# Kernel optimization log

Measured on AMD Instinct MI355X. Metric: run time of the kernel, lower is better.

Reference implementation:

```python
import jax, jax.numpy as jnp
import numpy as np

N_NODES = 100000
N_EDGES = 1600000
IN_CH = 128
HID = 128
OUT_DIM = 1
N_LAYERS = 3
N_GRAPHS = 512


def setup_inputs() -> dict:
    key = jax.random.key(0)
    ks = jax.random.split(key, 12)
    x = jax.random.normal(ks[0], (N_NODES, IN_CH), dtype=jnp.float32)
    edge_index = jax.random.randint(ks[1], (2, N_EDGES), 0, N_NODES, dtype=jnp.int64)
    batch = jnp.sort(jax.random.randint(ks[2], (N_NODES,), 0, N_GRAPHS, dtype=jnp.int64))
    # GCNConv weights (glorot) and biases; layer 0: in->hid, rest hid->hid (all 128x128 here)
    def glorot(k, fan_in, fan_out):
        lim = jnp.sqrt(6.0 / (fan_in + fan_out)).astype(jnp.float32)
        return jax.random.uniform(k, (fan_in, fan_out), jnp.float32, -lim, lim)
    Ws = jnp.stack([glorot(ks[3 + i], IN_CH if i == 0 else HID, HID) for i in range(N_LAYERS)])
    bs = jnp.zeros((N_LAYERS, HID), dtype=jnp.float32)
    head_w = glorot(ks[8], HID, OUT_DIM)  # stored as [hid, out] == head_weight.T
    head_b = jnp.zeros((OUT_DIM,), dtype=jnp.float32)
    return {"x": x, "edge_index": edge_index, "batch": batch,
            "Ws": Ws, "bs": bs, "head_w": head_w, "head_b": head_b}


def _gcn_norm(edge_index, n_nodes):
    # PyG gcn_norm: add self-loops, deg over dst, norm = d^-1/2[src]*d^-1/2[dst]
    loops = jnp.arange(n_nodes, dtype=edge_index.dtype)
    src = jnp.concatenate([edge_index[0], loops])
    dst = jnp.concatenate([edge_index[1], loops])
    deg = jax.ops.segment_sum(jnp.ones_like(dst, dtype=jnp.float32), dst, num_segments=n_nodes)
    dinv = jnp.where(deg > 0, jax.lax.rsqrt(deg), 0.0)
    norm = dinv[src] * dinv[dst]
    return src, dst, norm


def reference(x, edge_index, batch, Ws, bs, head_w, head_b):
    n = x.shape[0]
    src, dst, norm = _gcn_norm(edge_index, n)
    h = x.astype(jnp.float32)
    for i in range(N_LAYERS):
        t = h @ Ws[i]                                   # [N, hid]
        msg = t[src] * norm[:, None]                    # gather + scale [E+N, hid]
        h = jax.ops.segment_sum(msg, dst, num_segments=n) + bs[i]
        h = jax.nn.relu(h)                              # dropout p=0 -> identity
    g = jax.ops.segment_sum(h, batch, num_segments=N_GRAPHS)  # global_add_pool
    out = g @ head_w + head_b                           # [G, 1]
    return out.reshape(-1)                              # squeeze out_dim==1
```

## Files before the change

kernel.cpp:

```cpp
#include <hip/hip_runtime.h>

#define NN 100000
#define NE 1600000
#define CH 128
#define NG 512
#define NL 3
#define BSZ 512
#define NBUK ((NN + BSZ - 1) / BSZ)
#define TILE 4096

typedef short bf8 __attribute__((ext_vector_type(8)));
typedef float f4 __attribute__((ext_vector_type(4)));
typedef unsigned int u32x4 __attribute__((ext_vector_type(4)));
typedef unsigned short u16;
typedef unsigned int u32;

__device__ __forceinline__ long long ld_idx(const void* p, long long i, bool is64) {
    return is64 ? ((const long long*)p)[i] : (long long)((const int*)p)[i];
}
__device__ __forceinline__ u16 f2bf(float f) {
    u32 u = __float_as_uint(f);
    u += 0x7fffu + ((u >> 16) & 1u);
    return (u16)(u >> 16);
}
__device__ __forceinline__ float bflo(u32 v) { return __uint_as_float(v << 16); }
__device__ __forceinline__ float bfhi(u32 v) { return __uint_as_float(v & 0xffff0000u); }

__global__ void k_zero(int* bcnt, int* flags) {
    int i = blockIdx.x * blockDim.x + threadIdx.x;
    if (i < NBUK) bcnt[i] = 0;
    if (i < 2) flags[i] = 0;
}

__global__ void k_detect(const int* __restrict__ ei32, const int* __restrict__ b32, int* flags) {
    int acc_e = 0, acc_b = 0;
    long long stride = (long long)gridDim.x * blockDim.x;
    long long t0 = (long long)blockIdx.x * blockDim.x + threadIdx.x;
    for (long long i = t0; i < (1 << 18); i += stride) acc_e |= ei32[2 * i + 1];
    for (long long i = t0; i < NN / 2; i += stride) acc_b |= b32[2 * i + 1];
    if (acc_e) atomicOr(&flags[0], 1);
    if (acc_b) atomicOr(&flags[1], 1);
}


__global__ __launch_bounds__(256) void k_hist(const void* __restrict__ ei,
                                              const int* __restrict__ flags,
                                              int* __restrict__ bcnt) {
    __shared__ int cnt[NBUK];
    int tid = threadIdx.x;
    long long e0 = (long long)blockIdx.x * TILE;
    bool is64 = (flags[0] == 0);
    for (int b = tid; b < NBUK; b += 256) cnt[b] = 0;
    __syncthreads();
#pragma unroll
    for (int k = 0; k < 16; ++k) {
        long long e = e0 + tid + k * 256;
        if (e < NE) {
            int d = (int)ld_idx(ei, NE + e, is64);
            atomicAdd(&cnt[d >> 9], 1);
        }
    }
    __syncthreads();
    for (int b = tid; b < NBUK; b += 256)
        if (cnt[b]) atomicAdd(&bcnt[b], cnt[b]);
}

__global__ __launch_bounds__(256) void k_bscan(const int* __restrict__ bcnt,
                                               int* __restrict__ gbase,
                                               int* __restrict__ gcur,
                                               int* __restrict__ rowptr) {
    __shared__ int ws4[4];
    int t = threadIdx.x;
    int v = (t < NBUK) ? bcnt[t] : 0;
    int x = v;
#pragma unroll
    for (int d = 1; d < 64; d <<= 1) {
        int y = __shfl_up(x, d, 64);
        if ((t & 63) >= d) x += y;
    }
    if ((t & 63) == 63) ws4[t >> 6] = x;
    __syncthreads();
    if (t == 0) {
        int s = 0;
#pragma unroll
        for (int w = 0; w < 4; ++w) { int tmp = ws4[w]; ws4[w] = s; s += tmp; }
    }
    __syncthreads();
    int ex = x - v + ws4[t >> 6];
    if (t < NBUK) { gbase[t] = ex; gcur[t] = ex; }
    if (t == NBUK - 1) gbase[NBUK] = ex + v;
    if (t == 0) rowptr[NN] = NE;
}

__global__ __launch_bounds__(256) void k_bin(const void* __restrict__ ei,
                                             const int* __restrict__ flags,
                                             int* __restrict__ gcur,
                                             u32* __restrict__ bin) {
    __shared__ u32 stag[TILE];
    __shared__ int cnt[NBUK], loff[NBUK], lcur[NBUK], gb_s[NBUK];
    int tid = threadIdx.x;
    long long e0 = (long long)blockIdx.x * TILE;
    bool is64 = (flags[0] == 0);

    u32 rec[16];
    int bk[16];
#pragma unroll
    for (int k = 0; k < 16; ++k) {
        long long e = e0 + tid + k * 256;
        if (e < NE) {
            int s = (int)ld_idx(ei, e, is64);
            int d = (int)ld_idx(ei, NE + e, is64);
            rec[k] = ((u32)s << 9) | (u32)(d & (BSZ - 1));
            bk[k] = d >> 9;
        } else bk[k] = -1;
    }
    for (int b = tid; b < NBUK; b += 256) { cnt[b] = 0; lcur[b] = 0; }
    __syncthreads();
#pragma unroll
    for (int k = 0; k < 16; ++k)
        if (bk[k] >= 0) atomicAdd(&cnt[bk[k]], 1);
    __syncthreads();
    if (tid == 0) {
        int run = 0;
        for (int b = 0; b < NBUK; ++b) { loff[b] = run; run += cnt[b]; }
    }
    __syncthreads();
    if (tid < NBUK && cnt[tid] > 0) gb_s[tid] = atomicAdd(&gcur[tid], cnt[tid]);
    __syncthreads();
#pragma unroll
    for (int k = 0; k < 16; ++k)
        if (bk[k] >= 0) {
            int pos = loff[bk[k]] + atomicAdd(&lcur[bk[k]], 1);
            stag[pos] = rec[k];
        }
    __syncthreads();
    int wv = tid >> 6, lane = tid & 63;
    for (int b = wv; b < NBUK; b += 4) {
        int n = cnt[b];
        int gb = (n > 0) ? gb_s[b] : 0;
        int lo = loff[b];
        for (int j = lane; j < n; j += 64) bin[gb + j] = stag[lo + j];
    }
}

__global__ __launch_bounds__(512) void k_fillc(const u32* __restrict__ bin,
                                               const int* __restrict__ gbase,
                                               int* __restrict__ rowptr,
                                               float* __restrict__ dinv,
                                               u32* __restrict__ csr) {
    __shared__ int cnt[BSZ];
    __shared__ int lcur[BSZ];
    __shared__ int wsum[8];
    int b = blockIdx.x, tid = threadIdx.x;
    int gb = gbase[b], ge = gbase[b + 1];
    cnt[tid] = 0;
    __syncthreads();
    for (int i = gb + tid; i < ge; i += BSZ)
        atomicAdd(&cnt[bin[i] & (BSZ - 1)], 1);
    __syncthreads();
    int v = cnt[tid];
    int x = v;
#pragma unroll
    for (int d = 1; d < 64; d <<= 1) {
        int y = __shfl_up(x, d, 64);
        if ((tid & 63) >= d) x += y;
    }
    if ((tid & 63) == 63) wsum[tid >> 6] = x;
    __syncthreads();
    if (tid == 0) {
        int s = 0;
#pragma unroll
        for (int w = 0; w < 8; ++w) { int tmp = wsum[w]; wsum[w] = s; s += tmp; }
    }
    __syncthreads();
    int off = gb + x - v + wsum[tid >> 6];
    int node = b * BSZ + tid;
    if (node < NN) {
        rowptr[node] = off;
        dinv[node] = rsqrtf((float)v + 1.0f);
    }
    lcur[tid] = off;
    __syncthreads();
    for (int i = gb + tid; i < ge; i += BSZ) {
        u32 rec = bin[i];
        int pos = atomicAdd(&lcur[rec & (BSZ - 1)], 1);
        csr[pos] = rec >> 9;
    }
}

__global__ void k_cvt_w(const float* __restrict__ Ws, u16* __restrict__ Wt) {
    int j = (blockIdx.x * blockDim.x + threadIdx.x) * 4;
    if (j >= NL * CH * CH) return;
    int l = j >> 14, c = (j >> 7) & 127, k = j & 127;
    ushort4 o;
    o.x = f2bf(Ws[(l << 14) + ((k + 0) << 7) + c]);
    o.y = f2bf(Ws[(l << 14) + ((k + 1) << 7) + c]);
    o.z = f2bf(Ws[(l << 14) + ((k + 2) << 7) + c]);
    o.w = f2bf(Ws[(l << 14) + ((k + 3) << 7) + c]);
    *(ushort4*)(Wt + j) = o;
}

template <int F32IN>
__global__ __launch_bounds__(256) void k_mm_t(const void* __restrict__ Ain,
                                              const u16* __restrict__ Wt,
                                              u16* __restrict__ out) {
    int tid = threadIdx.x;
    int lane = tid & 63;
    int wv = tid >> 6;
    int rbase = blockIdx.x * 128 + wv * 32;
    int lm = lane & 15;
    int lk = (lane >> 4) << 3;

    f4 acc[2][8];
#pragma unroll
    for (int m = 0; m < 2; ++m)
#pragma unroll
        for (int n = 0; n < 8; ++n) acc[m][n] = (f4){0.f, 0.f, 0.f, 0.f};

    int r0 = rbase + lm;      if (r0 >= NN) r0 = NN - 1;
    int r1 = rbase + 16 + lm; if (r1 >= NN) r1 = NN - 1;

#pragma unroll
    for (int kk = 0; kk < 4; ++kk) {
        int ko = kk * 32 + lk;
        bf8 a0, a1;
        if (F32IN) {
            const float* A = (const float*)Ain;
            float4 p0 = *(const float4*)(A + (size_t)r0 * CH + ko);
            float4 q0 = *(const float4*)(A + (size_t)r0 * CH + ko + 4);
            float4 p1 = *(const float4*)(A + (size_t)r1 * CH + ko);
            float4 q1 = *(const float4*)(A + (size_t)r1 * CH + ko + 4);
            a0[0] = (short)f2bf(p0.x); a0[1] = (short)f2bf(p0.y);
            a0[2] = (short)f2bf(p0.z); a0[3] = (short)f2bf(p0.w);
            a0[4] = (short)f2bf(q0.x); a0[5] = (short)f2bf(q0.y);
            a0[6] = (short)f2bf(q0.z); a0[7] = (short)f2bf(q0.w);
            a1[0] = (short)f2bf(p1.x); a1[1] = (short)f2bf(p1.y);
            a1[2] = (short)f2bf(p1.z); a1[3] = (short)f2bf(p1.w);
            a1[4] = (short)f2bf(q1.x); a1[5] = (short)f2bf(q1.y);
            a1[6] = (short)f2bf(q1.z); a1[7] = (short)f2bf(q1.w);
        } else {
            const u16* A = (const u16*)Ain;
            a0 = *(const bf8*)(A + (size_t)r0 * CH + ko);
            a1 = *(const bf8*)(A + (size_t)r1 * CH + ko);
        }
#pragma unroll
        for (int n = 0; n < 8; ++n) {
            bf8 b = *(const bf8*)(Wt + (n * 16 + lm) * CH + ko);
            acc[0][n] = __builtin_amdgcn_mfma_f32_16x16x32_bf16(a0, b, acc[0][n], 0, 0, 0);
            acc[1][n] = __builtin_amdgcn_mfma_f32_16x16x32_bf16(a1, b, acc[1][n], 0, 0, 0);
        }
    }

#pragma unroll
    for (int m = 0; m < 2; ++m) {
        int rb = rbase + m * 16 + (lane >> 4) * 4;
#pragma unroll
        for (int r = 0; r < 4; ++r) {
            int row = rb + r;
            if (row < NN) {
#pragma unroll
                for (int n = 0; n < 8; ++n)
                    out[(size_t)row * CH + n * 16 + lm] = f2bf(acc[m][n][r]);
            }
        }
    }
}

#define ACC8W(v, w) \
    acc[0] = fmaf(bflo(v[0]), w, acc[0]); acc[1] = fmaf(bfhi(v[0]), w, acc[1]); \
    acc[2] = fmaf(bflo(v[1]), w, acc[2]); acc[3] = fmaf(bfhi(v[1]), w, acc[3]); \
    acc[4] = fmaf(bflo(v[2]), w, acc[4]); acc[5] = fmaf(bfhi(v[2]), w, acc[5]); \
    acc[6] = fmaf(bflo(v[3]), w, acc[6]); acc[7] = fmaf(bfhi(v[3]), w, acc[7]);

__global__ __launch_bounds__(256) void k_aggr(const u16* __restrict__ t,
                                              const int* __restrict__ rowptr,
                                              const u32* __restrict__ csr,
                                              const float* __restrict__ dinv,
                                              const float* __restrict__ b,
                                              u16* __restrict__ h,
                                              const float* __restrict__ hw,
                                              float* __restrict__ partial) {
    int node = blockIdx.x * 16 + (threadIdx.x >> 4);
    if (node >= NN) return;
    int l16 = threadIdx.x & 15;
    int c8 = l16 << 3;
    const u32x4* tp = (const u32x4*)t;

    int beg = rowptr[node], end = rowptr[node + 1];
    float dn = dinv[node];
    float acc[8];
#pragma unroll
    for (int k = 0; k < 8; ++k) acc[k] = 0.f;

    int j = beg;
    for (; j + 8 <= end; j += 8) {
        int s0 = (int)csr[j],     s1 = (int)csr[j + 1];
        int s2 = (int)csr[j + 2], s3 = (int)csr[j + 3];
        int s4 = (int)csr[j + 4], s5 = (int)csr[j + 5];
        int s6 = (int)csr[j + 6], s7 = (int)csr[j + 7];
        float w0 = dinv[s0], w1 = dinv[s1], w2 = dinv[s2], w3 = dinv[s3];
        float w4 = dinv[s4], w5 = dinv[s5], w6 = dinv[s6], w7 = dinv[s7];
        u32x4 v0 = tp[s0 * 16 + l16];
        u32x4 v1 = tp[s1 * 16 + l16];
        u32x4 v2 = tp[s2 * 16 + l16];
        u32x4 v3 = tp[s3 * 16 + l16];
        u32x4 v4 = tp[s4 * 16 + l16];
        u32x4 v5 = tp[s5 * 16 + l16];
        u32x4 v6 = tp[s6 * 16 + l16];
        u32x4 v7 = tp[s7 * 16 + l16];
        ACC8W(v0, w0); ACC8W(v1, w1); ACC8W(v2, w2); ACC8W(v3, w3);
        ACC8W(v4, w4); ACC8W(v5, w5); ACC8W(v6, w6); ACC8W(v7, w7);
    }
    for (; j + 4 <= end; j += 4) {
        int s0 = (int)csr[j], s1 = (int)csr[j + 1];
        int s2 = (int)csr[j + 2], s3 = (int)csr[j + 3];
        float w0 = dinv[s0], w1 = dinv[s1], w2 = dinv[s2], w3 = dinv[s3];
        u32x4 v0 = tp[s0 * 16 + l16];
        u32x4 v1 = tp[s1 * 16 + l16];
        u32x4 v2 = tp[s2 * 16 + l16];
        u32x4 v3 = tp[s3 * 16 + l16];
        ACC8W(v0, w0); ACC8W(v1, w1); ACC8W(v2, w2); ACC8W(v3, w3);
    }
    for (; j < end; ++j) {
        int s = (int)csr[j];
        float w = dinv[s];
        u32x4 v = tp[s * 16 + l16];
        ACC8W(v, w);
    }

    u32x4 sv = tp[node * 16 + l16];
    float4 b0 = *(const float4*)(b + c8);
    float4 b1 = *(const float4*)(b + c8 + 4);
    float r[8];
    r[0] = fmaxf(fmaf(fmaf(bflo(sv[0]), dn, acc[0]), dn, b0.x), 0.f);
    r[1] = fmaxf(fmaf(fmaf(bfhi(sv[0]), dn, acc[1]), dn, b0.y), 0.f);
    r[2] = fmaxf(fmaf(fmaf(bflo(sv[1]), dn, acc[2]), dn, b0.z), 0.f);
    r[3] = fmaxf(fmaf(fmaf(bfhi(sv[1]), dn, acc[3]), dn, b0.w), 0.f);
    r[4] = fmaxf(fmaf(fmaf(bflo(sv[2]), dn, acc[4]), dn, b1.x), 0.f);
    r[5] = fmaxf(fmaf(fmaf(bfhi(sv[2]), dn, acc[5]), dn, b1.y), 0.f);
    r[6] = fmaxf(fmaf(fmaf(bflo(sv[3]), dn, acc[6]), dn, b1.z), 0.f);
    r[7] = fmaxf(fmaf(fmaf(bfhi(sv[3]), dn, acc[7]), dn, b1.w), 0.f);

    if (hw) {
        float4 w0 = *(const float4*)(hw + c8);
        float4 w1 = *(const float4*)(hw + c8 + 4);
        float d = r[0] * w0.x + r[1] * w0.y + r[2] * w0.z + r[3] * w0.w
                + r[4] * w1.x + r[5] * w1.y + r[6] * w1.z + r[7] * w1.w;
#pragma unroll
        for (int off = 8; off > 0; off >>= 1) d += __shfl_xor(d, off);
        if (l16 == 0) partial[node] = d;
    } else {
        u32x4 o;
        o[0] = ((u32)f2bf(r[1]) << 16) | (u32)f2bf(r[0]);
        o[1] = ((u32)f2bf(r[3]) << 16) | (u32)f2bf(r[2]);
        o[2] = ((u32)f2bf(r[5]) << 16) | (u32)f2bf(r[4]);
        o[3] = ((u32)f2bf(r[7]) << 16) | (u32)f2bf(r[6]);
        ((u32x4*)h)[node * 16 + l16] = o;
    }
}


__device__ __forceinline__ int lbound(const void* bt, bool is64, int target) {
    int lo = 0, hi = NN;
    while (lo < hi) {
        int mid = (lo + hi) >> 1;
        long long v = ld_idx(bt, mid, is64);
        if (v < (long long)target) lo = mid + 1; else hi = mid;
    }
    return lo;
}

__global__ __launch_bounds__(256) void k_head(const float* __restrict__ partial,
                                              const void* __restrict__ batch,
                                              const int* __restrict__ flags,
                                              const float* __restrict__ hb,
                                              float* __restrict__ out) {
    int g = blockIdx.x * 4 + (threadIdx.x >> 6);
    if (g >= NG) return;
    int lane = threadIdx.x & 63;
    bool is64 = (flags[1] == 0);
    int lo = lbound(batch, is64, g);
    int hi = lbound(batch, is64, g + 1);
    float s = 0.f;
    for (int i = lo + lane; i < hi; i += 64) s += partial[i];
#pragma unroll
    for (int off = 32; off > 0; off >>= 1) s += __shfl_down(s, off);
    if (lane == 0) out[g] = s + hb[0];
}

extern "C" void kernel_launch(void* const* d_in, const int* in_sizes, int n_in,
                              void* d_out, int out_size, void* d_ws, size_t ws_size,
                              hipStream_t stream) {
    const float* x  = (const float*)d_in[0];
    const void*  ei = d_in[1];
    const void*  bt = d_in[2];
    const float* Ws = (const float*)d_in[3];
    const float* bs = (const float*)d_in[4];
    const float* hw = (const float*)d_in[5];
    const float* hb = (const float*)d_in[6];
    float* out = (float*)d_out;

    char* ws = (char*)d_ws;
    size_t p = 0;
    auto alloc = [&](size_t bytes) { size_t r = p; p += (bytes + 255) & ~(size_t)255; return r; };
    size_t o_flags  = alloc(256);
    size_t o_dinv   = alloc((size_t)NN * 4);
    size_t o_rowptr = alloc((size_t)(NN + 1) * 4);
    size_t o_bcnt   = alloc((size_t)NBUK * 4);
    size_t o_gbase  = alloc((size_t)(NBUK + 1) * 4);
    size_t o_gcur   = alloc((size_t)NBUK * 4);
    size_t o_part   = alloc((size_t)NN * 4);
    size_t o_bin    = alloc((size_t)NE * 4);
    size_t o_csr    = alloc((size_t)NE * 4);
    size_t o_tb     = alloc((size_t)NN * CH * 2);
    size_t o_hb     = alloc((size_t)NN * CH * 2);
    size_t o_wt     = alloc((size_t)NL * CH * CH * 2);
    (void)ws_size;

    int*   flags  = (int*)(ws + o_flags);
    float* dinv   = (float*)(ws + o_dinv);
    int*   rowptr = (int*)(ws + o_rowptr);
    int*   bcnt   = (int*)(ws + o_bcnt);
    int*   gbase  = (int*)(ws + o_gbase);
    int*   gcur   = (int*)(ws + o_gcur);
    float* part   = (float*)(ws + o_part);
    u32*   bin    = (u32*)(ws + o_bin);
    u32*   csr    = (u32*)(ws + o_csr);
    u16*   tb     = (u16*)(ws + o_tb);
    u16*   hbuf   = (u16*)(ws + o_hb);
    u16*   Wt     = (u16*)(ws + o_wt);

    k_zero<<<1, 256, 0, stream>>>(bcnt, flags);
    k_detect<<<256, 256, 0, stream>>>((const int*)ei, (const int*)bt, flags);
    k_hist<<<(NE + TILE - 1) / TILE, 256, 0, stream>>>(ei, flags, bcnt);
    k_bscan<<<1, 256, 0, stream>>>(bcnt, gbase, gcur, rowptr);
    k_bin<<<(NE + TILE - 1) / TILE, 256, 0, stream>>>(ei, flags, gcur, bin);
    k_fillc<<<NBUK, BSZ, 0, stream>>>(bin, gbase, rowptr, dinv, csr);
    k_cvt_w<<<(NL * CH * CH / 4 + 255) / 256, 256, 0, stream>>>(Ws, Wt);

    const void* hin = (const void*)x;
    for (int l = 0; l < NL; ++l) {
        bool last = (l == NL - 1);
        if (l == 0)
            k_mm_t<1><<<(NN + 127) / 128, 256, 0, stream>>>(hin, Wt, tb);
        else
            k_mm_t<0><<<(NN + 127) / 128, 256, 0, stream>>>(hin, Wt + (size_t)l * CH * CH, tb);
        k_aggr<<<(NN + 15) / 16, 256, 0, stream>>>(tb, rowptr, csr, dinv,
                                                   bs + (size_t)l * CH, hbuf,
                                                   last ? hw : nullptr, part);
        hin = (const void*)hbuf;
    }

    k_head<<<(NG + 3) / 4, 256, 0, stream>>>(part, bt, flags, hb, out);
}
```

Before: 367.1 us.

## Slice node features into 16-channel column panels for cache-local aggregation

Stores the intermediate features as 8 slices of 16 channels each ([slice][node][16] bf16), so each aggregation block gathers only a 32-byte slice per neighbour. Blocks are interleaved by slice, the intent being that one slice of the table (about 3.2MB) stays resident in L2/LLC during the random gather. The matmul reads and writes this sliced layout, and the head dot-product is split out of the last aggregation into a separate pooling kernel. The cost is that CSR indices and dinv are re-read once per slice (8x index traffic), each gather is a smaller transaction, and there is one extra kernel launch and pass over h.

```diff
diff --git a/kernel.cpp b/kernel.cpp
--- a/kernel.cpp
+++ b/kernel.cpp
@@ -12,6 +12,7 @@
 typedef short bf8 __attribute__((ext_vector_type(8)));
 typedef float f4 __attribute__((ext_vector_type(4)));
 typedef unsigned int u32x4 __attribute__((ext_vector_type(4)));
+typedef unsigned int u32x2 __attribute__((ext_vector_type(2)));
 typedef unsigned short u16;
 typedef unsigned int u32;
 
@@ -240,12 +241,13 @@
             a1[6] = (short)f2bf(q1.z); a1[7] = (short)f2bf(q1.w);
         } else {
             const u16* A = (const u16*)Ain;
-            a0 = *(const bf8*)(A + (size_t)r0 * CH + ko);
-            a1 = *(const bf8*)(A + (size_t)r1 * CH + ko);
+            int sl = ko >> 4, of = ko & 15;
+            a0 = *(const bf8*)(A + ((size_t)sl * NN + r0) * 16 + of);
+            a1 = *(const bf8*)(A + ((size_t)sl * NN + r1) * 16 + of);
         }
 #pragma unroll
         for (int n = 0; n < 8; ++n) {
-            bf8 b = *(const bf8*)(Wt + (n * 16 + lm) * CH + ko);
+            bf8 b = *(const bf8*)(Wt + (n * 16 + lm) * CH + kk * 32 + lk);
             acc[0][n] = __builtin_amdgcn_mfma_f32_16x16x32_bf16(a0, b, acc[0][n], 0, 0, 0);
             acc[1][n] = __builtin_amdgcn_mfma_f32_16x16x32_bf16(a1, b, acc[1][n], 0, 0, 0);
         }
@@ -260,103 +262,83 @@
             if (row < NN) {
 #pragma unroll
                 for (int n = 0; n < 8; ++n)
-                    out[(size_t)row * CH + n * 16 + lm] = f2bf(acc[m][n][r]);
+                    out[((size_t)n * NN + row) * 16 + lm] = f2bf(acc[m][n][r]);
             }
         }
     }
 }
 
-#define ACC8W(v, w) \
-    acc[0] = fmaf(bflo(v[0]), w, acc[0]); acc[1] = fmaf(bfhi(v[0]), w, acc[1]); \
-    acc[2] = fmaf(bflo(v[1]), w, acc[2]); acc[3] = fmaf(bfhi(v[1]), w, acc[3]); \
-    acc[4] = fmaf(bflo(v[2]), w, acc[4]); acc[5] = fmaf(bfhi(v[2]), w, acc[5]); \
-    acc[6] = fmaf(bflo(v[3]), w, acc[6]); acc[7] = fmaf(bfhi(v[3]), w, acc[7]);
-
-__global__ __launch_bounds__(256) void k_aggr(const u16* __restrict__ t,
+__global__ __launch_bounds__(256) void k_aggr(const u32* __restrict__ tsl,
                                               const int* __restrict__ rowptr,
                                               const u32* __restrict__ csr,
                                               const float* __restrict__ dinv,
                                               const float* __restrict__ b,
-                                              u16* __restrict__ h,
-                                              const float* __restrict__ hw,
-                                              float* __restrict__ partial) {
+                                              u32* __restrict__ hsl) {
+    int s = blockIdx.x & 7;
+    int node = (blockIdx.x >> 3) * 64 + (threadIdx.x >> 2);
+    if (node >= NN) return;
+    int l4 = threadIdx.x & 3;
+    const u32* tb = tsl + (size_t)s * NN * 8;
+    int beg = rowptr[node], end = rowptr[node + 1];
+    float dn = dinv[node];
+    float a0 = 0.f, a1 = 0.f, a2 = 0.f, a3 = 0.f;
+
+    int j = beg;
+    for (; j + 4 <= end; j += 4) {
+        int s0 = (int)csr[j],     s1 = (int)csr[j + 1];
+        int s2 = (int)csr[j + 2], s3 = (int)csr[j + 3];
+        float w0 = dinv[s0], w1 = dinv[s1], w2 = dinv[s2], w3 = dinv[s3];
+        u32x2 v0 = *(const u32x2*)(tb + s0 * 8 + l4 * 2);
+        u32x2 v1 = *(const u32x2*)(tb + s1 * 8 + l4 * 2);
+        u32x2 v2 = *(const u32x2*)(tb + s2 * 8 + l4 * 2);
+        u32x2 v3 = *(const u32x2*)(tb + s3 * 8 + l4 * 2);
+        a0 = fmaf(bflo(v0[0]), w0, a0); a1 = fmaf(bfhi(v0[0]), w0, a1);
+        a2 = fmaf(bflo(v0[1]), w0, a2); a3 = fmaf(bfhi(v0[1]), w0, a3);
+        a0 = fmaf(bflo(v1[0]), w1, a0); a1 = fmaf(bfhi(v1[0]), w1, a1);
+        a2 = fmaf(bflo(v1[1]), w1, a2); a3 = fmaf(bfhi(v1[1]), w1, a3);
+        a0 = fmaf(bflo(v2[0]), w2, a0); a1 = fmaf(bfhi(v2[0]), w2, a1);
+        a2 = fmaf(bflo(v2[1]), w2, a2); a3 = fmaf(bfhi(v2[1]), w2, a3);
+        a0 = fmaf(bflo(v3[0]), w3, a0); a1 = fmaf(bfhi(v3[0]), w3, a1);
+        a2 = fmaf(bflo(v3[1]), w3, a2); a3 = fmaf(bfhi(v3[1]), w3, a3);
+    }
+    for (; j < end; ++j) {
+        int s0 = (int)csr[j];
+        float w0 = dinv[s0];
+        u32x2 v0 = *(const u32x2*)(tb + s0 * 8 + l4 * 2);
+        a0 = fmaf(bflo(v0[0]), w0, a0); a1 = fmaf(bfhi(v0[0]), w0, a1);
+        a2 = fmaf(bflo(v0[1]), w0, a2); a3 = fmaf(bfhi(v0[1]), w0, a3);
+    }
+
+    u32x2 sv = *(const u32x2*)(tb + node * 8 + l4 * 2);
+    float4 bv = *(const float4*)(b + s * 16 + l4 * 4);
+    float r0 = fmaxf(fmaf(fmaf(bflo(sv[0]), dn, a0), dn, bv.x), 0.f);
+    float r1 = fmaxf(fmaf(fmaf(bfhi(sv[0]), dn, a1), dn, bv.y), 0.f);
+    float r2 = fmaxf(fmaf(fmaf(bflo(sv[1]), dn, a2), dn, bv.z), 0.f);
+    float r3 = fmaxf(fmaf(fmaf(bfhi(sv[1]), dn, a3), dn, bv.w), 0.f);
+    u32x2 o;
+    o[0] = ((u32)f2bf(r1) << 16) | (u32)f2bf(r0);
+    o[1] = ((u32)f2bf(r3) << 16) | (u32)f2bf(r2);
+    *(u32x2*)(hsl + (size_t)s * NN * 8 + node * 8 + l4 * 2) = o;
+}
+
+__global__ __launch_bounds__(256) void k_poolh(const u32* __restrict__ hsl,
+                                               const float* __restrict__ hw,
+                                               float* __restrict__ partial) {
     int node = blockIdx.x * 16 + (threadIdx.x >> 4);
     if (node >= NN) return;
-    int l16 = threadIdx.x & 15;
-    int c8 = l16 << 3;
-    const u32x4* tp = (const u32x4*)t;
-
-    int beg = rowptr[node], end = rowptr[node + 1];
-    float dn = dinv[node];
-    float acc[8];
-#pragma unroll
-    for (int k = 0; k < 8; ++k) acc[k] = 0.f;
-
-    int j = beg;
-    for (; j + 8 <= end; j += 8) {
-        int s0 = (int)csr[j],     s1 = (int)csr[j + 1];
-        int s2 = (int)csr[j + 2], s3 = (int)csr[j + 3];
-        int s4 = (int)csr[j + 4], s5 = (int)csr[j + 5];
-        int s6 = (int)csr[j + 6], s7 = (int)csr[j + 7];
-        float w0 = dinv[s0], w1 = dinv[s1], w2 = dinv[s2], w3 = dinv[s3];
-        float w4 = dinv[s4], w5 = dinv[s5], w6 = dinv[s6], w7 = dinv[s7];
-        u32x4 v0 = tp[s0 * 16 + l16];
-        u32x4 v1 = tp[s1 * 16 + l16];
-        u32x4 v2 = tp[s2 * 16 + l16];
-        u32x4 v3 = tp[s3 * 16 + l16];
-        u32x4 v4 = tp[s4 * 16 + l16];
-        u32x4 v5 = tp[s5 * 16 + l16];
-        u32x4 v6 = tp[s6 * 16 + l16];
-        u32x4 v7 = tp[s7 * 16 + l16];
-        ACC8W(v0, w0); ACC8W(v1, w1); ACC8W(v2, w2); ACC8W(v3, w3);
-        ACC8W(v4, w4); ACC8W(v5, w5); ACC8W(v6, w6); ACC8W(v7, w7);
-    }
-    for (; j + 4 <= end; j += 4) {
-        int s0 = (int)csr[j], s1 = (int)csr[j + 1];
-        int s2 = (int)csr[j + 2], s3 = (int)csr[j + 3];
-        float w0 = dinv[s0], w1 = dinv[s1], w2 = dinv[s2], w3 = dinv[s3];
-        u32x4 v0 = tp[s0 * 16 + l16];
-        u32x4 v1 = tp[s1 * 16 + l16];
-        u32x4 v2 = tp[s2 * 16 + l16];
-        u32x4 v3 = tp[s3 * 16 + l16];
-        ACC8W(v0, w0); ACC8W(v1, w1); ACC8W(v2, w2); ACC8W(v3, w3);
-    }
-    for (; j < end; ++j) {
-        int s = (int)csr[j];
-        float w = dinv[s];
-        u32x4 v = tp[s * 16 + l16];
-        ACC8W(v, w);
-    }
-
-    u32x4 sv = tp[node * 16 + l16];
-    float4 b0 = *(const float4*)(b + c8);
-    float4 b1 = *(const float4*)(b + c8 + 4);
-    float r[8];
-    r[0] = fmaxf(fmaf(fmaf(bflo(sv[0]), dn, acc[0]), dn, b0.x), 0.f);
-    r[1] = fmaxf(fmaf(fmaf(bfhi(sv[0]), dn, acc[1]), dn, b0.y), 0.f);
-    r[2] = fmaxf(fmaf(fmaf(bflo(sv[1]), dn, acc[2]), dn, b0.z), 0.f);
-    r[3] = fmaxf(fmaf(fmaf(bfhi(sv[1]), dn, acc[3]), dn, b0.w), 0.f);
-    r[4] = fmaxf(fmaf(fmaf(bflo(sv[2]), dn, acc[4]), dn, b1.x), 0.f);
-    r[5] = fmaxf(fmaf(fmaf(bfhi(sv[2]), dn, acc[5]), dn, b1.y), 0.f);
-    r[6] = fmaxf(fmaf(fmaf(bflo(sv[3]), dn, acc[6]), dn, b1.z), 0.f);
-    r[7] = fmaxf(fmaf(fmaf(bfhi(sv[3]), dn, acc[7]), dn, b1.w), 0.f);
-
-    if (hw) {
-        float4 w0 = *(const float4*)(hw + c8);
-        float4 w1 = *(const float4*)(hw + c8 + 4);
-        float d = r[0] * w0.x + r[1] * w0.y + r[2] * w0.z + r[3] * w0.w
-                + r[4] * w1.x + r[5] * w1.y + r[6] * w1.z + r[7] * w1.w;
-#pragma unroll
-        for (int off = 8; off > 0; off >>= 1) d += __shfl_xor(d, off);
-        if (l16 == 0) partial[node] = d;
-    } else {
-        u32x4 o;
-        o[0] = ((u32)f2bf(r[1]) << 16) | (u32)f2bf(r[0]);
-        o[1] = ((u32)f2bf(r[3]) << 16) | (u32)f2bf(r[2]);
-        o[2] = ((u32)f2bf(r[5]) << 16) | (u32)f2bf(r[4]);
-        o[3] = ((u32)f2bf(r[7]) << 16) | (u32)f2bf(r[6]);
-        ((u32x4*)h)[node * 16 + l16] = o;
-    }
+    int l = threadIdx.x & 15;
+    int sl = l >> 1, half = l & 1;
+    const u32* p = hsl + ((size_t)sl * NN + node) * 8 + half * 4;
+    u32x4 v = *(const u32x4*)p;
+    float4 w0 = *(const float4*)(hw + sl * 16 + half * 8);
+    float4 w1 = *(const float4*)(hw + sl * 16 + half * 8 + 4);
+    float d = bflo(v[0]) * w0.x + bfhi(v[0]) * w0.y
+            + bflo(v[1]) * w0.z + bfhi(v[1]) * w0.w
+            + bflo(v[2]) * w1.x + bfhi(v[2]) * w1.y
+            + bflo(v[3]) * w1.z + bfhi(v[3]) * w1.w;
+#pragma unroll
+    for (int off = 8; off > 0; off >>= 1) d += __shfl_xor(d, off);
+    if (l == 0) partial[node] = d;
 }
 
 
@@ -438,18 +420,18 @@
     k_fillc<<<NBUK, BSZ, 0, stream>>>(bin, gbase, rowptr, dinv, csr);
     k_cvt_w<<<(NL * CH * CH / 4 + 255) / 256, 256, 0, stream>>>(Ws, Wt);
 
+    const int aggr_blocks = ((NN + 63) / 64) * 8;
     const void* hin = (const void*)x;
     for (int l = 0; l < NL; ++l) {
-        bool last = (l == NL - 1);
         if (l == 0)
             k_mm_t<1><<<(NN + 127) / 128, 256, 0, stream>>>(hin, Wt, tb);
         else
             k_mm_t<0><<<(NN + 127) / 128, 256, 0, stream>>>(hin, Wt + (size_t)l * CH * CH, tb);
-        k_aggr<<<(NN + 15) / 16, 256, 0, stream>>>(tb, rowptr, csr, dinv,
-                                                   bs + (size_t)l * CH, hbuf,
-                                                   last ? hw : nullptr, part);
+        k_aggr<<<aggr_blocks, 256, 0, stream>>>((const u32*)tb, rowptr, csr, dinv,
+                                                bs + (size_t)l * CH, (u32*)hbuf);
         hin = (const void*)hbuf;
     }
 
+    k_poolh<<<(NN + 15) / 16, 256, 0, stream>>>((const u32*)hbuf, hw, part);
     k_head<<<(NG + 3) / 4, 256, 0, stream>>>(part, bt, flags, hb, out);
 }
```

After: 584.0 us. +59.1%, slower.
